# Optimization experiments

Hardware: AMD Instinct MI355X
Metric: run time of the kernel (lower is better)

Reference implementation:

```python
import jax, jax.numpy as jnp
import numpy as np

NUM_EXPERTS = 8
TOP_K = 2
HIDDEN = 2048
INTER = 5632
NUM_TOKENS = 8192


def setup_inputs() -> dict:
    key = jax.random.key(0)
    ks = jax.random.split(key, 5)
    s_h = 1.0 / np.sqrt(HIDDEN)
    s_i = 1.0 / np.sqrt(INTER)
    return {
        "hidden_states": jax.random.normal(ks[0], (NUM_TOKENS, HIDDEN), jnp.float32),
        # router: ReplicatedLinear(hidden, num_experts, bias=False) -> weight [E, H]
        "w_router": jax.random.normal(ks[1], (NUM_EXPERTS, HIDDEN), jnp.float32) * s_h,
        # FusedMoE SiLU-gated MLP per expert: gate/up [E, H, I], down [E, I, H]
        "w_gate": jax.random.normal(ks[2], (NUM_EXPERTS, HIDDEN, INTER), jnp.float32) * s_h,
        "w_up": jax.random.normal(ks[3], (NUM_EXPERTS, HIDDEN, INTER), jnp.float32) * s_h,
        "w_down": jax.random.normal(ks[4], (NUM_EXPERTS, INTER, HIDDEN), jnp.float32) * s_i,
    }


def reference(hidden_states, w_router, w_gate, w_up, w_down):
    x = hidden_states  # [T, H]
    # Router linear (no bias)
    router_logits = x @ w_router.T  # [T, E]
    # FusedMoE topk: softmax over all experts, take top-k, renormalize=False
    probs = jax.nn.softmax(router_logits.astype(jnp.float32), axis=-1)
    topk_w, topk_idx = jax.lax.top_k(probs, TOP_K)  # [T, k]
    topk_w = topk_w.astype(x.dtype)

    out = jnp.zeros_like(x)
    for e in range(NUM_EXPERTS):
        # combine weight for tokens that routed to expert e (0 otherwise)
        w_e = jnp.sum(jnp.where(topk_idx == e, topk_w, 0.0), axis=-1)  # [T]
        h = jax.nn.silu(x @ w_gate[e]) * (x @ w_up[e])  # [T, I]
        out = out + (h @ w_down[e]) * w_e[:, None]
    return out
```

## Files before the change

### kernel.cpp

```cpp
#include <hip/hip_runtime.h>
#include <hip/hip_bf16.h>
#include <cstdint>

#define NTOK 8192
#define NEXP 8
#define HID  2048
#define INTR 5632
#define NT1  44
#define NT2  16

#define TCNT_OFF    4096u
#define SLOT_OFF    65536u
#define T2S_OFF     262144u
#define W2_OFF      393216u
#define LISTS_OFF   524288u
#define WL_OFF      786432u
#define WG_OFF      2097152u
#define WBYTES      184549376u
#define WU_OFF      (WG_OFF + WBYTES)
#define HF_OFF      (WU_OFF + WBYTES)
#define HFBYTES     207618048u
#define XG_OFF      (HF_OFF + HFBYTES)

typedef float f32x4  __attribute__((ext_vector_type(4)));
typedef short s16x8  __attribute__((ext_vector_type(8)));
typedef short s16x4  __attribute__((ext_vector_type(4)));

__device__ __forceinline__ short bfc(float f) {
  __hip_bfloat16 h = __float2bfloat16(f);
  return __builtin_bit_cast(short, h);
}
__device__ __forceinline__ float b2f(short s) {
  unsigned u = ((unsigned)(unsigned short)s) << 16;
  return __builtin_bit_cast(float, u);
}
__device__ __forceinline__ s16x8 pk8(float4 a, float4 b) {
  s16x8 v;
  v[0]=bfc(a.x); v[1]=bfc(a.y); v[2]=bfc(a.z); v[3]=bfc(a.w);
  v[4]=bfc(b.x); v[5]=bfc(b.y); v[6]=bfc(b.z); v[7]=bfc(b.w);
  return v;
}
__device__ __forceinline__ void gload16(const void* g, void* l) {
  __builtin_amdgcn_global_load_lds((const __attribute__((address_space(1))) void*)g,
                                   (__attribute__((address_space(3))) void*)l, 16, 0, 0);
}

#define DSR128(dst, addr, IMM) \
  asm volatile("ds_read_b128 %0, %1 offset:" IMM : "=v"(dst) : "v"(addr))
#define DSW128(addr, data, IMM) \
  asm volatile("ds_write_b128 %0, %1 offset:" IMM :: "v"(addr), "v"(data))
#define WAITLGKM(N) do { \
  asm volatile("s_waitcnt lgkmcnt(" #N ")" ::: "memory"); \
  __builtin_amdgcn_sched_barrier(0); } while (0)
#define WAITVM(N) do { \
  asm volatile("s_waitcnt vmcnt(" #N ")" ::: "memory"); \
  __builtin_amdgcn_sched_barrier(0); } while (0)

#define LOADA4(D0, D1, D2, D3, PTR) \
  asm volatile("global_load_dwordx4 %0, %4, off\n\t" \
               "global_load_dwordx4 %1, %4, off offset:1024\n\t" \
               "global_load_dwordx4 %2, %4, off offset:2048\n\t" \
               "global_load_dwordx4 %3, %4, off offset:3072" \
               : "=&v"(D0), "=&v"(D1), "=&v"(D2), "=&v"(D3) : "v"(PTR))
#define LOADB2(DG, DU, PG, PU) \
  asm volatile("global_load_dwordx4 %0, %2, off\n\t" \
               "global_load_dwordx4 %1, %3, off" \
               : "=&v"(DG), "=&v"(DU) : "v"(PG), "v"(PU))

#define MFMA_BF16 __builtin_amdgcn_mfma_f32_16x16x32_bf16

__global__ __launch_bounds__(256, 4) void prep_kernel(
    const float* __restrict__ src, short* __restrict__ dst,
    int KT, int NP, int Nsrc) {
  __shared__ float tile[32 * 132];
  const int b = blockIdx.x;
  const int np = b % NP;
  const int kt = (b / NP) % KT;
  const int e  = b / (NP * KT);
  const int tid = threadIdx.x;
  const float* s = src + (size_t)e * KT * 32 * (size_t)Nsrc + (size_t)kt * 32 * Nsrc + np * 128;
#pragma unroll
  for (int i = 0; i < 4; i++) {
    const int idx = tid + i * 256;
    const int row = idx >> 5, c4 = idx & 31;
    float4 v = *(const float4*)(s + (size_t)row * Nsrc + c4 * 4);
    *(float4*)(tile + row * 132 + c4 * 4) = v;
  }
  __syncthreads();
  short* dbase = dst + ((size_t)(e * KT + kt) * (NP * 8) + np * 8) * 512;
#pragma unroll
  for (int i = 0; i < 2; i++) {
    const int c = tid + i * 256;
    const int lane = c & 63;
    const int nf = c >> 6;
    const int n = nf * 16 + (lane & 15);
    const int kb = (lane >> 4) * 8;
    s16x8 o;
#pragma unroll
    for (int j = 0; j < 8; j++) o[j] = bfc(tile[(kb + j) * 132 + n]);
    *(s16x8*)(dbase + (size_t)c * 8) = o;
  }
}

__global__ void router_kernel(const float* __restrict__ x, const float* __restrict__ wr,
                              int* __restrict__ cnt, int* __restrict__ lists,
                              float* __restrict__ wlists) {
  const int wave = threadIdx.x >> 6;
  const int lane = threadIdx.x & 63;
  const int t = blockIdx.x * 4 + wave;
  if (t >= NTOK) return;
  float acc[NEXP];
#pragma unroll
  for (int e = 0; e < NEXP; e++) acc[e] = 0.f;
  const float* xrow = x + (size_t)t * HID;
#pragma unroll
  for (int j = 0; j < HID / 256; j++) {
    const int k = j * 256 + lane * 4;
    float4 xv = *(const float4*)(xrow + k);
#pragma unroll
    for (int e = 0; e < NEXP; e++) {
      float4 wv = *(const float4*)(wr + e * HID + k);
      acc[e] += xv.x * wv.x + xv.y * wv.y + xv.z * wv.z + xv.w * wv.w;
    }
  }
#pragma unroll
  for (int e = 0; e < NEXP; e++) {
    float v = acc[e];
    for (int off = 32; off; off >>= 1) v += __shfl_xor(v, off, 64);
    acc[e] = v;
  }
  if (lane == 0) {
    float m = acc[0];
#pragma unroll
    for (int e = 1; e < NEXP; e++) m = fmaxf(m, acc[e]);
    float p[NEXP], s = 0.f;
#pragma unroll
    for (int e = 0; e < NEXP; e++) { p[e] = __expf(acc[e] - m); s += p[e]; }
    const float inv = 1.f / s;
    int e1 = 0; float b1 = p[0];
#pragma unroll
    for (int e = 1; e < NEXP; e++) if (p[e] > b1) { b1 = p[e]; e1 = e; }
    int e2 = -1; float b2 = -1.f;
#pragma unroll
    for (int e = 0; e < NEXP; e++) if (e != e1 && p[e] > b2) { b2 = p[e]; e2 = e; }
    const int pos1 = atomicAdd(&cnt[e1], 1);
    lists[e1 * NTOK + pos1] = t; wlists[e1 * NTOK + pos1] = b1 * inv;
    const int pos2 = atomicAdd(&cnt[e2], 1);
    lists[e2 * NTOK + pos2] = t; wlists[e2 * NTOK + pos2] = b2 * inv;
  }
}

__global__ void offsets_kernel(const int* __restrict__ cnt, int* __restrict__ poffs) {
  if (threadIdx.x == 0 && blockIdx.x == 0) {
    int o = 0;
#pragma unroll
    for (int e = 0; e < NEXP; e++) { poffs[e] = o; o += ((cnt[e] + 255) >> 8) << 8; }
    poffs[NEXP] = o;
  }
}

__global__ void slotmap_kernel(const int* __restrict__ cnt, const int* __restrict__ poffs,
                               const int* __restrict__ lists, const float* __restrict__ wlists,
                               int* __restrict__ slotlist, int* __restrict__ tcnt,
                               int* __restrict__ tok2slot, float* __restrict__ w2) {
  const int e = blockIdx.x;
  const int c = cnt[e], base = poffs[e];
  for (int pos = threadIdx.x; pos < c; pos += blockDim.x) {
    const int tok = lists[e * NTOK + pos];
    const int slot = base + pos;
    slotlist[slot] = tok;
    const int j = atomicAdd(&tcnt[tok], 1);
    tok2slot[tok * 2 + j] = slot;
    w2[tok * 2 + j] = wlists[e * NTOK + pos];
  }
}

__global__ __launch_bounds__(256, 4) void gather_kernel(
    const float* __restrict__ x, const int* __restrict__ slotlist,
    short* __restrict__ xg) {
  const int c = blockIdx.x * 256 + threadIdx.x;
  const int cl = c & 63;
  const int fragid = c >> 6;
  const int f = fragid & 15;
  const int kt = (fragid >> 4) & 63;
  const int gmt = fragid >> 10;
  const int tok = slotlist[gmt * 256 + f * 16 + (cl & 15)];
  const float* s = x + (size_t)tok * HID + kt * 32 + (cl >> 4) * 8;
  float4 a = *(const float4*)s, b = *(const float4*)(s + 4);
  *(s16x8*)(xg + (size_t)c * 8) = pk8(a, b);
}

__global__ __launch_bounds__(512, 2) void gemm1_kernel(
    const short* __restrict__ xg, const short* __restrict__ wgb,
    const short* __restrict__ wub, const int* __restrict__ cnt,
    const int* __restrict__ poffs, short* __restrict__ hfrag) {
  const int P = blockIdx.x;
  const int xcd = P & 7, slot = P >> 3;
  const int mt = slot & 31, jj = slot >> 5;
  const int g = jj * 8 + xcd;
  const int e = g / NT1, nt = g % NT1;
  if (mt * 256 >= cnt[e]) return;
  const int gmt = (poffs[e] >> 8) + mt;
  const int tid = threadIdx.x;
  const int w = tid >> 6, lane = tid & 63;
  const int wm = w >> 1, wn = w & 1;

  __shared__ __align__(16) short Lds[34816];
  const uint32_t ldsbase = (uint32_t)(uintptr_t)&Lds[0];

  const short* srcA  = xg + (size_t)gmt * 64 * 16 * 512 + (size_t)(wm * 4) * 512 + lane * 8;
  const short* srcBg = wgb + (((size_t)e * 64) * 352 + nt * 8) * 512 + tid * 8;
  const short* srcBu = wub + (((size_t)e * 64) * 352 + nt * 8) * 512 + tid * 8;

  const uint32_t roB = wn * 4096 + lane * 16;
  const uint32_t roU = 8192 + wn * 4096 + lane * 16;
  const uint32_t awr = ldsbase + tid * 16;

  f32x4 accG[4][4], accU[4][4];
#pragma unroll
  for (int i = 0; i < 4; i++)
#pragma unroll
    for (int j = 0; j < 4; j++) {
      accG[i][j] = f32x4{0.f, 0.f, 0.f, 0.f};
      accU[i][j] = f32x4{0.f, 0.f, 0.f, 0.f};
    }

  s16x8 arA0, arA1, arA2, arA3, arB0, arB1, arB2, arB3;
  s16x8 g0p, u0p, g1p, u1p;

  LOADB2(g0p, u0p, srcBg, srcBu); srcBg += 180224; srcBu += 180224;
  LOADA4(arA0, arA1, arA2, arA3, srcA); srcA += 8192;
  LOADB2(g1p, u1p, srcBg, srcBu); srcBg += 180224; srcBu += 180224;
  WAITVM(6);
  DSW128(awr, g0p, "0");
  DSW128(awr, u0p, "8192");
  WAITLGKM(0);

#define MMQ(NF, BG, BU, A0, A1, A2, A3)                                         \
  { __builtin_amdgcn_s_setprio(1);                                              \
    accG[0][NF] = MFMA_BF16(A0, BG, accG[0][NF], 0, 0, 0);                      \
    accU[0][NF] = MFMA_BF16(A0, BU, accU[0][NF], 0, 0, 0);                      \
    accG[1][NF] = MFMA_BF16(A1, BG, accG[1][NF], 0, 0, 0);                      \
    accU[1][NF] = MFMA_BF16(A1, BU, accU[1][NF], 0, 0, 0);                      \
    accG[2][NF] = MFMA_BF16(A2, BG, accG[2][NF], 0, 0, 0);                      \
    accU[2][NF] = MFMA_BF16(A2, BU, accU[2][NF], 0, 0, 0);                      \
    accG[3][NF] = MFMA_BF16(A3, BG, accG[3][NF], 0, 0, 0);                      \
    accU[3][NF] = MFMA_BF16(A3, BU, accU[3][NF], 0, 0, 0);                      \
    __builtin_amdgcn_s_setprio(0); }

#define G1_BODY(RBOFF, WIG, WIU, U0,U1,U2,U3, L0,L1,L2,L3, WPG,WPU, LPG,LPU,    \
                VTOP, DO_A, DO_WR, DO_LB, LGA, LGB, LGC, LGD)                   \
  {                                                                             \
    WAITVM(VTOP);                                       \
    __builtin_amdgcn_s_barrier();                     \
    const uint32_t rb = ldsbase + (RBOFF);                                      \
    s16x8 bg0, bg1, bg2, bg3, bu0, bu1, bu2, bu3;                               \
    DSR128(bg0, rb + roB, "0");    DSR128(bu0, rb + roU, "0");                  \
    DSR128(bg1, rb + roB, "1024"); DSR128(bu1, rb + roU, "1024");               \
    DSR128(bg2, rb + roB, "2048"); DSR128(bu2, rb + roU, "2048");               \
    DSR128(bg3, rb + roB, "3072"); DSR128(bu3, rb + roU, "3072");               \
    if (DO_A) { LOADA4(L0, L1, L2, L3, srcA); srcA += 8192; }                   \
    if (DO_WR) {                                                                \
      WAITVM(4);                                     \
      DSW128(awr, WPG, WIG);                                                    \
      DSW128(awr, WPU, WIU);                                                    \
    }                                                                           \
    if (DO_LB) { LOADB2(LPG, LPU, srcBg, srcBu);                                \
                 srcBg += 180224; srcBu += 180224; }                            \
    WAITLGKM(LGA);                                                              \
    MMQ(0, bg0, bu0, U0, U1, U2, U3)                                            \
    WAITLGKM(LGB);                                                              \
    MMQ(1, bg1, bu1, U0, U1, U2, U3)                                            \
    WAITLGKM(LGC);                                                              \
    MMQ(2, bg2, bu2, U0, U1, U2, U3)                                            \
    WAITLGKM(LGD);                                                              \
    MMQ(3, bg3, bu3, U0, U1, U2, U3)                                            \
    WAITLGKM(0);                         \
  }

  for (int it = 0; it < 31; ++it) {
    G1_BODY(0,     "16384","24576", arA0,arA1,arA2,arA3, arB0,arB1,arB2,arB3,
            g1p,u1p, g0p,u0p, 2, 1, 1, 1, 8, 6, 4, 2)
    G1_BODY(16384, "0","8192",      arB0,arB1,arB2,arB3, arA0,arA1,arA2,arA3,
            g0p,u0p, g1p,u1p, 2, 1, 1, 1, 8, 6, 4, 2)
  }
  G1_BODY(0,     "16384","24576", arA0,arA1,arA2,arA3, arB0,arB1,arB2,arB3,
          g1p,u1p, g0p,u0p, 2, 1, 1, 0, 8, 6, 4, 2)
  G1_BODY(16384, "0","8192",      arB0,arB1,arB2,arB3, arA0,arA1,arA2,arA3,
          g0p,u0p, g1p,u1p, 0, 0, 0, 0, 6, 4, 2, 0)
#undef G1_BODY
#undef MMQ

  short* tr = (short*)Lds;
  __syncthreads();
#pragma unroll
  for (int mf = 0; mf < 4; mf++)
#pragma unroll
    for (int reg = 0; reg < 4; reg++) {
      const int row = wm * 64 + mf * 16 + (lane >> 4) * 4 + reg;
#pragma unroll
      for (int nf = 0; nf < 4; nf++) {
        const int col = wn * 64 + nf * 16 + (lane & 15);
        const float gv = accG[mf][nf][reg];
        const float uv = accU[mf][nf][reg];
        tr[row * 136 + col] = bfc((gv / (1.f + __expf(-gv))) * uv);
      }
    }
  __syncthreads();
  short* hb = hfrag + (((size_t)gmt * 176 + nt * 4) * 16) * 512;
#pragma unroll
  for (int i = 0; i < 8; i++) {
    const int c = tid + i * 512;
    const int cl = c & 63;
    const int f = (c >> 6) & 15;
    const int ktl = c >> 10;
    const int rr = f * 16 + (cl & 15);
    s16x8 v = *(const s16x8*)(tr + rr * 136 + ktl * 32 + (cl >> 4) * 8);
    *(s16x8*)(hb + ((size_t)ktl * 16 + f) * 512 + cl * 8) = v;
  }
}

__global__ __launch_bounds__(512, 4) void gemm2_kernel(
    const short* __restrict__ hfrag, const short* __restrict__ wdb,
    const int* __restrict__ cnt, const int* __restrict__ poffs,
    __hip_bfloat16* __restrict__ pout) {
  const int P = blockIdx.x;
  const int xcd = P & 7, r = P >> 3;
  const int nt = r & 15, emq = r >> 4;
  const int gm = emq * 8 + xcd;
  const int e = gm >> 5, mt = gm & 31;
  if (mt * 256 >= cnt[e]) return;
  const int gmt = (poffs[e] >> 8) + mt;
  const int n0 = nt * 128;
  const int tid = threadIdx.x;
  const int w = tid >> 6, lane = tid & 63;
  const int wm = w >> 1, wn = w & 1;

  __shared__ __align__(16) short Lds[3 * 12288];
  const uint32_t ldsbase = (uint32_t)(uintptr_t)&Lds[0];

  const short* srcA = hfrag + (size_t)gmt * 176 * 16 * 512 + tid * 8;
  const short* srcB = wdb + (((size_t)e * 176) * 128 + nt * 8) * 512 + tid * 8;

  const uint32_t roA = wm * 4096 + lane * 16;
  const uint32_t roB = 16384 + wn * 4096 + lane * 16;

  f32x4 acc[4][4];
#pragma unroll
  for (int i = 0; i < 4; i++)
#pragma unroll
    for (int j = 0; j < 4; j++) acc[i][j] = f32x4{0.f, 0.f, 0.f, 0.f};

#define STG2(WB) do {                                                           \
    short* d = (short*)Lds + ((WB) >> 1);                                       \
    gload16(srcA,        d + w * 512);                                          \
    gload16(srcA + 4096, d + 4096 + w * 512);                                   \
    gload16(srcB,        d + 8192 + w * 512);                                   \
    srcA += 8192; srcB += 65536; } while (0)

#define MMQ2(NF, BF)                                                            \
  { __builtin_amdgcn_s_setprio(1);                                              \
    acc[0][NF] = MFMA_BF16(af0, BF, acc[0][NF], 0, 0, 0);                       \
    acc[1][NF] = MFMA_BF16(af1, BF, acc[1][NF], 0, 0, 0);                       \
    acc[2][NF] = MFMA_BF16(af2, BF, acc[2][NF], 0, 0, 0);                       \
    acc[3][NF] = MFMA_BF16(af3, BF, acc[3][NF], 0, 0, 0);                       \
    __builtin_amdgcn_s_setprio(0); }

#define G2_BODY(RB, WB, VMN, DOSTG)                                             \
  {                                                                             \
    WAITVM(VMN);                                                                \
    __builtin_amdgcn_s_barrier();                                               \
    const uint32_t rb = ldsbase + (RB);                                         \
    s16x8 af0, af1, af2, af3, bf0, bf1, bf2, bf3;                               \
    DSR128(bf0, rb + roB, "0");                                                 \
    DSR128(af0, rb + roA, "0");    DSR128(af1, rb + roA, "1024");               \
    DSR128(af2, rb + roA, "2048"); DSR128(af3, rb + roA, "3072");               \
    DSR128(bf1, rb + roB, "1024");                                              \
    DSR128(bf2, rb + roB, "2048");                                              \
    DSR128(bf3, rb + roB, "3072");                                              \
    if (DOSTG) { STG2(WB); }                                                    \
    WAITLGKM(3);                                                                \
    MMQ2(0, bf0)                                                                \
    WAITLGKM(2);                                                                \
    MMQ2(1, bf1)                                                                \
    WAITLGKM(1);                                                                \
    MMQ2(2, bf2)                                                                \
    WAITLGKM(0);                                                                \
    MMQ2(3, bf3)                                                                \
  }

  STG2(0);
  STG2(24576);
  for (int it = 0; it < 58; ++it) {
    G2_BODY(0,     49152, 3, 1)
    G2_BODY(24576, 0,     3, 1)
    G2_BODY(49152, 24576, 3, 1)
  }
  G2_BODY(0,     0, 3, 0)
  G2_BODY(24576, 0, 0, 0)
#undef G2_BODY
#undef MMQ2
#undef STG2

  const int slotb = poffs[e] + mt * 256;
#pragma unroll
  for (int mf = 0; mf < 4; mf++) {
#pragma unroll
    for (int reg = 0; reg < 4; reg++) {
      const int row = wm * 64 + mf * 16 + (lane >> 4) * 4 + reg;
      __hip_bfloat16* op = pout + (size_t)(slotb + row) * HID + n0 + wn * 64 + (lane & 15);
#pragma unroll
      for (int nf = 0; nf < 4; nf++)
        op[nf * 16] = __float2bfloat16(acc[mf][nf][reg]);
    }
  }
}

__global__ __launch_bounds__(256, 8) void combine_kernel(
    const __hip_bfloat16* __restrict__ pout, const int* __restrict__ tok2slot,
    const float* __restrict__ w2, float* __restrict__ out) {
  const int t = blockIdx.x;
  const int s0 = tok2slot[2 * t], s1 = tok2slot[2 * t + 1];
  const float w0 = w2[2 * t], w1 = w2[2 * t + 1];
  const short* p0 = (const short*)pout + (size_t)s0 * HID;
  const short* p1 = (const short*)pout + (size_t)s1 * HID;
  float* o = out + (size_t)t * HID;
  const int i = threadIdx.x;
  s16x8 a = *(const s16x8*)(p0 + i * 8);
  s16x8 b = *(const s16x8*)(p1 + i * 8);
  float4 r0, r1;
  r0.x = w0 * b2f(a[0]) + w1 * b2f(b[0]);
  r0.y = w0 * b2f(a[1]) + w1 * b2f(b[1]);
  r0.z = w0 * b2f(a[2]) + w1 * b2f(b[2]);
  r0.w = w0 * b2f(a[3]) + w1 * b2f(b[3]);
  r1.x = w0 * b2f(a[4]) + w1 * b2f(b[4]);
  r1.y = w0 * b2f(a[5]) + w1 * b2f(b[5]);
  r1.z = w0 * b2f(a[6]) + w1 * b2f(b[6]);
  r1.w = w0 * b2f(a[7]) + w1 * b2f(b[7]);
  *(float4*)(o + i * 8) = r0;
  *(float4*)(o + i * 8 + 4) = r1;
}

extern "C" void kernel_launch(void* const* d_in, const int* in_sizes, int n_in,
                              void* d_out, int out_size, void* d_ws, size_t ws_size,
                              hipStream_t stream) {
  const float* x  = (const float*)d_in[0];
  const float* wr = (const float*)d_in[1];
  const float* wg = (const float*)d_in[2];
  const float* wu = (const float*)d_in[3];
  const float* wd = (const float*)d_in[4];
  float* out = (float*)d_out;
  char* ws = (char*)d_ws;

  int* cnt      = (int*)ws;
  int* poffs    = (int*)(ws + 64);
  int* tcnt     = (int*)(ws + TCNT_OFF);
  int* slotlist = (int*)(ws + SLOT_OFF);
  int* tok2slot = (int*)(ws + T2S_OFF);
  float* w2     = (float*)(ws + W2_OFF);
  int* lists    = (int*)(ws + LISTS_OFF);
  float* wlists = (float*)(ws + WL_OFF);
  short* wgb    = (short*)(ws + WG_OFF);
  short* wub    = (short*)(ws + WU_OFF);
  short* wdb    = (short*)(ws + WG_OFF);
  short* hfrag  = (short*)(ws + HF_OFF);
  short* xg     = (short*)(ws + XG_OFF);
  __hip_bfloat16* pout = (__hip_bfloat16*)(ws + XG_OFF);

  hipMemsetAsync(ws, 0, 256, stream);
  hipMemsetAsync(ws + TCNT_OFF, 0, 32768, stream);
  hipMemsetAsync(ws + SLOT_OFF, 0, 73728, stream);

  router_kernel<<<NTOK / 4, 256, 0, stream>>>(x, wr, cnt, lists, wlists);
  offsets_kernel<<<1, 64, 0, stream>>>(cnt, poffs);
  slotmap_kernel<<<NEXP, 256, 0, stream>>>(cnt, poffs, lists, wlists, slotlist, tcnt, tok2slot, w2);
  gather_kernel<<<18432, 256, 0, stream>>>(x, slotlist, xg);
  prep_kernel<<<NEXP * 64 * 44, 256, 0, stream>>>(wg, wgb, 64, 44, INTR);
  prep_kernel<<<NEXP * 64 * 44, 256, 0, stream>>>(wu, wub, 64, 44, INTR);
  gemm1_kernel<<<8 * 32 * NT1, 512, 0, stream>>>(xg, wgb, wub, cnt, poffs, hfrag);
  prep_kernel<<<NEXP * 176 * 16, 256, 0, stream>>>(wd, wdb, 176, 16, HID);
  gemm2_kernel<<<8 * 16 * 32, 512, 0, stream>>>(hfrag, wdb, cnt, poffs, pout);
  combine_kernel<<<NTOK, 256, 0, stream>>>(pout, tok2slot, w2, out);
}
```

Measured before the change: 1.780 ms.

## Stage gate/up weights via direct global-to-LDS loads with triple buffering

The gate/up GEMM's B-operand staging now uses global_load_lds to copy weight tiles straight into shared memory, instead of loading them into registers and writing them with ds_write. The LDS ring grows from two buffers to three, and the main loop is unrolled by six with new vmcnt/lgkmcnt wait points. This is meant to remove register pressure and LDS write instructions and to deepen prefetch. It relies on the three-stage ring offsets and wait counts staying correct, and it uses more LDS.

```diff
diff --git a/kernel.cpp b/kernel.cpp
--- a/kernel.cpp
+++ b/kernel.cpp
@@ -47,8 +47,6 @@
 
 #define DSR128(dst, addr, IMM) \
   asm volatile("ds_read_b128 %0, %1 offset:" IMM : "=v"(dst) : "v"(addr))
-#define DSW128(addr, data, IMM) \
-  asm volatile("ds_write_b128 %0, %1 offset:" IMM :: "v"(addr), "v"(data))
 #define WAITLGKM(N) do { \
   asm volatile("s_waitcnt lgkmcnt(" #N ")" ::: "memory"); \
   __builtin_amdgcn_sched_barrier(0); } while (0)
@@ -62,10 +60,6 @@
                "global_load_dwordx4 %2, %4, off offset:2048\n\t" \
                "global_load_dwordx4 %3, %4, off offset:3072" \
                : "=&v"(D0), "=&v"(D1), "=&v"(D2), "=&v"(D3) : "v"(PTR))
-#define LOADB2(DG, DU, PG, PU) \
-  asm volatile("global_load_dwordx4 %0, %2, off\n\t" \
-               "global_load_dwordx4 %1, %3, off" \
-               : "=&v"(DG), "=&v"(DU) : "v"(PG), "v"(PU))
 
 #define MFMA_BF16 __builtin_amdgcn_mfma_f32_16x16x32_bf16
 
@@ -214,7 +208,6 @@
 
   const uint32_t roB = wn * 4096 + lane * 16;
   const uint32_t roU = 8192 + wn * 4096 + lane * 16;
-  const uint32_t awr = ldsbase + tid * 16;
 
   f32x4 accG[4][4], accU[4][4];
 #pragma unroll
@@ -226,17 +219,14 @@
     }
 
   s16x8 arA0, arA1, arA2, arA3, arB0, arB1, arB2, arB3;
-  s16x8 g0p, u0p, g1p, u1p;
-
-  LOADB2(g0p, u0p, srcBg, srcBu); srcBg += 180224; srcBu += 180224;
-  LOADA4(arA0, arA1, arA2, arA3, srcA); srcA += 8192;
-  LOADB2(g1p, u1p, srcBg, srcBu); srcBg += 180224; srcBu += 180224;
-  WAITVM(6);
-  DSW128(awr, g0p, "0");
-  DSW128(awr, u0p, "8192");
-  WAITLGKM(0);
-
-#define MMQ(NF, BG, BU, A0, A1, A2, A3)                                         \
+
+#define STG1(WB) do {                                                           \
+    short* d = (short*)Lds + ((WB) >> 1);                                       \
+    gload16(srcBg, d + w * 512);                                                \
+    gload16(srcBu, d + 4096 + w * 512);                                         \
+    srcBg += 180224; srcBu += 180224; } while (0)
+
+#define MMQ1(NF, BG, BU, A0, A1, A2, A3)                                        \
   { __builtin_amdgcn_s_setprio(1);                                              \
     accG[0][NF] = MFMA_BF16(A0, BG, accG[0][NF], 0, 0, 0);                      \
     accU[0][NF] = MFMA_BF16(A0, BU, accU[0][NF], 0, 0, 0);                      \
@@ -248,48 +238,48 @@
     accU[3][NF] = MFMA_BF16(A3, BU, accU[3][NF], 0, 0, 0);                      \
     __builtin_amdgcn_s_setprio(0); }
 
-#define G1_BODY(RBOFF, WIG, WIU, U0,U1,U2,U3, L0,L1,L2,L3, WPG,WPU, LPG,LPU,    \
-                VTOP, DO_A, DO_WR, DO_LB, LGA, LGB, LGC, LGD)                   \
+#define G1_BODY(RB, WB, U0, U1, U2, U3, L0, L1, L2, L3, VTOP, VMID, DO_A, DO_STG) \
   {                                                                             \
-    WAITVM(VTOP);                                       \
-    __builtin_amdgcn_s_barrier();                     \
-    const uint32_t rb = ldsbase + (RBOFF);                                      \
+    WAITVM(VTOP);                                                               \
+    __builtin_amdgcn_s_barrier();                                               \
+    const uint32_t rb = ldsbase + (RB);                                         \
     s16x8 bg0, bg1, bg2, bg3, bu0, bu1, bu2, bu3;                               \
     DSR128(bg0, rb + roB, "0");    DSR128(bu0, rb + roU, "0");                  \
     DSR128(bg1, rb + roB, "1024"); DSR128(bu1, rb + roU, "1024");               \
     DSR128(bg2, rb + roB, "2048"); DSR128(bu2, rb + roU, "2048");               \
     DSR128(bg3, rb + roB, "3072"); DSR128(bu3, rb + roU, "3072");               \
     if (DO_A) { LOADA4(L0, L1, L2, L3, srcA); srcA += 8192; }                   \
-    if (DO_WR) {                                                                \
-      WAITVM(4);                                     \
-      DSW128(awr, WPG, WIG);                                                    \
-      DSW128(awr, WPU, WIU);                                                    \
-    }                                                                           \
-    if (DO_LB) { LOADB2(LPG, LPU, srcBg, srcBu);                                \
-                 srcBg += 180224; srcBu += 180224; }                            \
-    WAITLGKM(LGA);                                                              \
-    MMQ(0, bg0, bu0, U0, U1, U2, U3)                                            \
-    WAITLGKM(LGB);                                                              \
-    MMQ(1, bg1, bu1, U0, U1, U2, U3)                                            \
-    WAITLGKM(LGC);                                                              \
-    MMQ(2, bg2, bu2, U0, U1, U2, U3)                                            \
-    WAITLGKM(LGD);                                                              \
-    MMQ(3, bg3, bu3, U0, U1, U2, U3)                                            \
-    WAITLGKM(0);                         \
-  }
-
-  for (int it = 0; it < 31; ++it) {
-    G1_BODY(0,     "16384","24576", arA0,arA1,arA2,arA3, arB0,arB1,arB2,arB3,
-            g1p,u1p, g0p,u0p, 2, 1, 1, 1, 8, 6, 4, 2)
-    G1_BODY(16384, "0","8192",      arB0,arB1,arB2,arB3, arA0,arA1,arA2,arA3,
-            g0p,u0p, g1p,u1p, 2, 1, 1, 1, 8, 6, 4, 2)
-  }
-  G1_BODY(0,     "16384","24576", arA0,arA1,arA2,arA3, arB0,arB1,arB2,arB3,
-          g1p,u1p, g0p,u0p, 2, 1, 1, 0, 8, 6, 4, 2)
-  G1_BODY(16384, "0","8192",      arB0,arB1,arB2,arB3, arA0,arA1,arA2,arA3,
-          g0p,u0p, g1p,u1p, 0, 0, 0, 0, 6, 4, 2, 0)
+    if (DO_STG) { STG1(WB); }                                                   \
+    WAITVM(VMID);                                                               \
+    WAITLGKM(6);                                                                \
+    MMQ1(0, bg0, bu0, U0, U1, U2, U3)                                           \
+    WAITLGKM(4);                                                                \
+    MMQ1(1, bg1, bu1, U0, U1, U2, U3)                                           \
+    WAITLGKM(2);                                                                \
+    MMQ1(2, bg2, bu2, U0, U1, U2, U3)                                           \
+    WAITLGKM(0);                                                                \
+    MMQ1(3, bg3, bu3, U0, U1, U2, U3)                                           \
+  }
+
+  STG1(0);
+  LOADA4(arA0, arA1, arA2, arA3, srcA); srcA += 8192;
+  STG1(16384);
+
+  for (int it = 0; it < 10; ++it) {
+    G1_BODY(0,     32768, arA0,arA1,arA2,arA3, arB0,arB1,arB2,arB3, 6, 8, 1, 1)
+    G1_BODY(16384, 0,     arB0,arB1,arB2,arB3, arA0,arA1,arA2,arA3, 6, 8, 1, 1)
+    G1_BODY(32768, 16384, arA0,arA1,arA2,arA3, arB0,arB1,arB2,arB3, 6, 8, 1, 1)
+    G1_BODY(0,     32768, arB0,arB1,arB2,arB3, arA0,arA1,arA2,arA3, 6, 8, 1, 1)
+    G1_BODY(16384, 0,     arA0,arA1,arA2,arA3, arB0,arB1,arB2,arB3, 6, 8, 1, 1)
+    G1_BODY(32768, 16384, arB0,arB1,arB2,arB3, arA0,arA1,arA2,arA3, 6, 8, 1, 1)
+  }
+  G1_BODY(0,     32768, arA0,arA1,arA2,arA3, arB0,arB1,arB2,arB3, 6, 8, 1, 1)
+  G1_BODY(16384, 0,     arB0,arB1,arB2,arB3, arA0,arA1,arA2,arA3, 6, 8, 1, 1)
+  G1_BODY(32768, 0,     arA0,arA1,arA2,arA3, arB0,arB1,arB2,arB3, 6, 6, 1, 0)
+  G1_BODY(0,     0,     arB0,arB1,arB2,arB3, arA0,arA1,arA2,arA3, 4, 0, 0, 0)
 #undef G1_BODY
-#undef MMQ
+#undef MMQ1
+#undef STG1
 
   short* tr = (short*)Lds;
   __syncthreads();
```

Result: faster. 1.677 ms (-5.8%).
